# Kernel tuning notes

Measured on AMD Instinct MI355X. Metric: run time of the kernel, lower is better.

## Reference

```python
import jax, jax.numpy as jnp
import numpy as np

T1 = -0.075410217
T2 = 0.0
T3 = 0.062207676


def my_squash2(s_j):
    # s_j: [B, 1, C, O, 1]; piecewise-linear rescale based on sorted channel-0 magnitudes.
    B, _, C, O, _ = s_j.shape
    f = s_j[:, 0, :, 0, 0]                      # [B, C] first element of each capsule
    order = jnp.argsort(f, axis=1)
    srt = jnp.take_along_axis(f, order, axis=1)  # ascending sort per sample
    i1 = jnp.sum(srt < T1, axis=1, keepdims=True)
    i2 = jnp.sum(srt < T2, axis=1, keepdims=True)
    i3 = jnp.sum(srt < T3, axis=1, keepdims=True)
    pos = jnp.arange(C)[None, :]
    seg1 = -0.074520095 * srt + 0.349297946
    seg2 = -0.534473989 * srt + 0.27196494
    seg3 = 0.637642944 * srt + 0.295330779
    seg4 = 0.169344703 * srt + 0.353784456
    # faithful to torch slices [0:i1-1], [i1:i2-1], [i2:i3-1], [i3:9] (segment-end indices untouched)
    m1 = (i1 > 0) & (pos < i1 - 1)
    m2 = (i2 > 0) & (i2 > i1) & (pos >= i1) & (pos < i2 - 1)
    m3 = (i3 > 0) & (i3 > i2) & (pos >= i2) & (pos < i3 - 1)
    m4 = (i3 < C) & (pos >= i3) & (pos < C - 1)
    new_srt = jnp.where(m1, seg1, jnp.where(m2, seg2, jnp.where(m3, seg3, jnp.where(m4, seg4, srt))))
    inv = jnp.argsort(order, axis=1)
    new_f = jnp.take_along_axis(new_srt, inv, axis=1)  # unsort back to capsule order
    # torch code mutates s_j in place: channel 0 of each capsule becomes new_f
    s_mut = s_j.at[:, 0, :, 0, 0].set(new_f)
    scale = new_f[:, None, :, None, None]            # expanded over out_channels
    return scale * s_mut, s_mut


def setup_inputs() -> dict:
    key = jax.random.key(0)
    k0, k1, k2, k3 = jax.random.split(key, 4)
    B, R, C, O, I = 100, 1152, 10, 16, 8
    return {
        "x0": jax.random.normal(k0, (B, R, I), dtype=jnp.float32),
        "x1": jax.random.normal(k1, (B, R, I), dtype=jnp.float32),
        "x2": jax.random.normal(k2, (B, 1, 28, 28), dtype=jnp.float32),
        "W": jax.random.normal(k3, (1, R, C, O, I), dtype=jnp.float32),
        "train_or_test": 0,
        "epch": 0,
    }


def reference(x0, x1, x2, W, train_or_test, epch):
    B, R, I = x0.shape
    C, O = W.shape[2], W.shape[3]
    squashed_u = jnp.broadcast_to(x0[:, :, None, :, None], (B, R, C, I, 1))
    # u_hat[b,r,c,o] = sum_i W[0,r,c,o,i] * x0[b,r,i]
    u_hat = jnp.einsum('rcoi,bri->brco', W[0], x0)[..., None]  # [B,R,C,O,1]
    b_ij = jnp.zeros((1, R, C, 1), dtype=x0.dtype)
    num_iterations = 3
    for it in range(num_iterations):
        c_ij = jax.nn.softmax(b_ij, axis=1)                    # over routes
        c_full = jnp.broadcast_to(c_ij, (B, R, C, 1))[..., None]
        s_j = jnp.sum(c_full * u_hat, axis=1, keepdims=True)   # [B,1,C,O,1]
        v_j, s_mut = my_squash2(s_j)
        if it < num_iterations - 1:
            a = jnp.einsum('brco,bco->brc', u_hat[..., 0], v_j[:, 0, :, :, 0])
            b_ij = b_ij + jnp.mean(a, axis=0)[None, :, :, None]
    Wb = jnp.broadcast_to(W, (B,) + W.shape[1:])
    return (v_j[:, 0], c_full, Wb, squashed_u, x1, x2, s_mut[:, 0])
```

## Files before the change

kernel.cpp:

```cpp
#include <hip/hip_runtime.h>

#define B 100
#define R 1152
#define C 10
#define O 16
#define I 8
#define RI 9216
#define RC2 2304
#define RCHUNK 16
#define NRC 72
#define KCH 128

#define T1c (-0.075410217f)
#define T3c (0.062207676f)

typedef float f4raw __attribute__((ext_vector_type(4)));
static __device__ __forceinline__ void nt_store4(const float4& v, float4* p) {
    __builtin_nontemporal_store(*(const f4raw*)&v, (f4raw*)p);
}

#define WS_BCOL 0
#define WS_CSM  11520
#define WS_PART 23040
#define WS_VOB  1175040
#define WS_VBCO 1191040
#define WS_SMUT 1207040

#define O_VJ 0
#define O_CF 4000
#define O_WB 292000
#define O_SQ 37156000
#define O_X1 39460000
#define O_X2 39690400
#define O_SM 39710000

#define U_WB 7200
#define U_SQ 563
#define U_X1 57
#define U_X2 5
#define U_TOT 7825

__device__ void stream_unit(int u, const float4* __restrict__ W4,
                            const float4* __restrict__ x04,
                            const float4* __restrict__ x14,
                            const float4* __restrict__ x24,
                            float4* __restrict__ out) {
    const int t = threadIdx.x;
    if (u < U_WB) {
        int wchunk = u % 1440, bg = u / 1440;
        int idx = wchunk * 256 + t;
        float4 v = W4[idx];
        float4* dst = out + O_WB + (size_t)bg * 20 * 368640 + idx;
        #pragma unroll
        for (int b = 0; b < 20; b++) { nt_store4(v, dst); dst += 368640; }
    } else if (u < U_WB + U_SQ) {
        int s = u - U_WB;
        int m0 = s * 4096, m1 = m0 + 4096; if (m1 > 2304000) m1 = 2304000;
        for (int m = m0 + t; m < m1; m += 256) {
            float4 v = x04[(m / 20) * 2 + (m & 1)];
            nt_store4(v, &out[O_SQ + m]);
        }
    } else if (u < U_WB + U_SQ + U_X1) {
        int s = u - U_WB - U_SQ;
        int m0 = s * 4096, m1 = m0 + 4096; if (m1 > 230400) m1 = 230400;
        for (int m = m0 + t; m < m1; m += 256) nt_store4(x14[m], &out[O_X1 + m]);
    } else {
        int s = u - U_WB - U_SQ - U_X1;
        int m0 = s * 4096, m1 = m0 + 4096; if (m1 > 19600) m1 = 19600;
        for (int m = m0 + t; m < m1; m += 256) nt_store4(x24[m], &out[O_X2 + m]);
    }
}

__global__ __launch_bounds__(256) void k_gemm(const float* __restrict__ Wg,
                                              const float* __restrict__ x0,
                                              float* __restrict__ ws,
                                              const float4* __restrict__ x14,
                                              const float4* __restrict__ x24,
                                              float4* __restrict__ out,
                                              int it, int ubase) {
    const int t = threadIdx.x;
    const float4* x04 = (const float4*)x0;
    if (blockIdx.x >= 720) {
        int k = blockIdx.x - 720;
        #pragma unroll 1
        for (int n = 0; n < 3; n++)
            stream_unit(ubase + k * 3 + n, (const float4*)Wg, x04, x14, x24, out);
        return;
    }
    const int rc = blockIdx.x % NRC, c = blockIdx.x / NRC;
    const int r0 = rc * RCHUNK;
    __shared__ float red[256];
    __shared__ float cw[RCHUNK];
    __shared__ __align__(16) float lw[KCH * O];
    __shared__ float tp[64][104];

    if (it > 0) {
        const float* bcol = ws + WS_BCOL + c * R;
        float lm = -3.4e38f;
        for (int r = t; r < R; r += 256) lm = fmaxf(lm, bcol[r]);
        red[t] = lm; __syncthreads();
        for (int s = 128; s > 0; s >>= 1) { if (t < s) red[t] = fmaxf(red[t], red[t + s]); __syncthreads(); }
        const float m = red[0]; __syncthreads();
        float ls = 0.f;
        for (int r = t; r < R; r += 256) ls += expf(bcol[r] - m);
        red[t] = ls; __syncthreads();
        for (int s = 128; s > 0; s >>= 1) { if (t < s) red[t] += red[t + s]; __syncthreads(); }
        const float sinv = 1.f / red[0];
        if (t < RCHUNK) cw[t] = expf(bcol[r0 + t] - m) * sinv;
        if (it == 2 && rc == 0) {
            for (int r = t; r < R; r += 256)
                ws[WS_CSM + r * C + c] = expf(bcol[r] - m) * sinv;
        }
    } else {
        if (t < RCHUNK) cw[t] = 1.0f / 1152.0f;
    }
    __syncthreads();

    for (int j = t; j < KCH * O; j += 256) {
        int rr = j >> 7;
        int rem = j & 127;
        int o = rem >> 3, i = rem & 7;
        lw[((rr * I + i) << 4) + o] = cw[rr] * Wg[((size_t)(r0 + rr) * C + c) * 128 + rem];
    }

    const int bl = t & 63, og = t >> 6;
    int b2 = bl + 64; if (b2 > 103) b2 = 103;
    float4 a0 = {0, 0, 0, 0}, a1 = {0, 0, 0, 0};
    for (int p = 0; p < 2; p++) {
        __syncthreads();
        int colbase = r0 * 2 + p * 16;
        for (int e = t; e < 1600; e += 256) {
            int b = e >> 4, q = e & 15;
            float4 v = x04[(size_t)b * RC2 + colbase + q];
            tp[q * 4 + 0][b] = v.x; tp[q * 4 + 1][b] = v.y;
            tp[q * 4 + 2][b] = v.z; tp[q * 4 + 3][b] = v.w;
        }
        tp[t >> 2][100 + (t & 3)] = 0.f;
        __syncthreads();
        const float4* lwp = (const float4*)lw + p * 64 * 4;
        #pragma unroll 8
        for (int k = 0; k < 64; k++) {
            float xv0 = tp[k][bl];
            float xv1 = tp[k][b2];
            float4 wv = lwp[k * 4 + og];
            a0.x += xv0 * wv.x; a0.y += xv0 * wv.y; a0.z += xv0 * wv.z; a0.w += xv0 * wv.w;
            a1.x += xv1 * wv.x; a1.y += xv1 * wv.y; a1.z += xv1 * wv.z; a1.w += xv1 * wv.w;
        }
    }
    float4* part4 = (float4*)(ws + WS_PART);
    int base = ((c * NRC + rc) * B + bl) * 4 + og;
    part4[base] = a0;
    if (bl < 36) part4[base + 64 * 4] = a1;
}

__global__ __launch_bounds__(256) void k_squash(float* __restrict__ ws,
                                                const float* __restrict__ Wg,
                                                const float* __restrict__ x0,
                                                const float4* __restrict__ x14,
                                                const float4* __restrict__ x24,
                                                float4* __restrict__ out, int ubase) {
    const int t = threadIdx.x;
    if (blockIdx.x >= B) {
        int k = blockIdx.x - B;
        #pragma unroll 1
        for (int n = 0; n < 2; n++)
            stream_unit(ubase + k * 2 + n, (const float4*)Wg, (const float4*)x0, x14, x24, out);
        return;
    }
    const int b = blockIdx.x;
    __shared__ float sl[160];
    __shared__ float nf[C];
    if (t < 160) {
        int c = t >> 4, o = t & 15;
        float s = 0.f;
        const float* p = ws + WS_PART + ((size_t)c * NRC * B + b) * 16 + o;
        #pragma unroll 8
        for (int rc = 0; rc < NRC; rc++) s += p[rc * 1600];
        sl[t] = s;
    }
    __syncthreads();
    if (t < C) {
        float fv[C];
        #pragma unroll
        for (int c2 = 0; c2 < C; c2++) fv[c2] = sl[c2 * O];
        float mine = sl[t * O];
        int rank = 0, i1 = 0, i2 = 0, i3 = 0;
        #pragma unroll
        for (int c2 = 0; c2 < C; c2++) {
            rank += (fv[c2] < mine) || (fv[c2] == mine && c2 < t);
            i1 += fv[c2] < T1c;
            i2 += fv[c2] < 0.0f;
            i3 += fv[c2] < T3c;
        }
        float nv = mine;
        if (i1 > 0 && rank < i1 - 1)                               nv = -0.074520095f * mine + 0.349297946f;
        else if (i2 > 0 && i2 > i1 && rank >= i1 && rank < i2 - 1) nv = -0.534473989f * mine + 0.27196494f;
        else if (i3 > 0 && i3 > i2 && rank >= i2 && rank < i3 - 1) nv = 0.637642944f * mine + 0.295330779f;
        else if (i3 < C && rank >= i3 && rank < C - 1)             nv = 0.169344703f * mine + 0.353784456f;
        nf[t] = nv;
    }
    __syncthreads();
    if (t < 160) {
        int c = t >> 4, o = t & 15;
        float sv = sl[t];
        float nfv = nf[c];
        float smut = (o == 0) ? nfv : sv;
        float v = nfv * smut;
        ws[WS_VBCO + b * 160 + t] = v;
        ws[WS_SMUT + b * 160 + t] = smut;
        ws[WS_VOB + t * B + b] = v;
    }
}

__global__ __launch_bounds__(256) void k_agree(const float* __restrict__ Wg,
                                               const float* __restrict__ x0,
                                               float* __restrict__ ws,
                                               const float4* __restrict__ x14,
                                               const float4* __restrict__ x24,
                                               float4* __restrict__ out,
                                               int it, int ubase) {
    const int t = threadIdx.x;
    if (blockIdx.x >= R) {
        int k = blockIdx.x - R;
        #pragma unroll 1
        for (int n = 0; n < 3; n++)
            stream_unit(ubase + k * 3 + n, (const float4*)Wg, (const float4*)x0, x14, x24, out);
        return;
    }
    const int r = blockIdx.x;
    __shared__ __align__(16) float vt[3200];
    __shared__ __align__(16) float xs[800];
    __shared__ __align__(16) float arr[1280];
    const float4* x04 = (const float4*)x0;
    if (t < 200) {
        int b = t >> 1, half = t & 1;
        float4 v = x04[(size_t)b * RC2 + r * 2 + half];
        xs[(half * 4 + 0) * B + b] = v.x; xs[(half * 4 + 1) * B + b] = v.y;
        xs[(half * 4 + 2) * B + b] = v.z; xs[(half * 4 + 3) * B + b] = v.w;
    }
    const int i = t & 7, co0 = t >> 3;
    const float4* xs4 = (const float4*)(xs + i * B);
    const float4* vt4 = (const float4*)(vt + co0 * B);
    for (int ch = 0; ch < 5; ch++) {
        __syncthreads();
        for (int j = t; j < 3200; j += 256) vt[j] = ws[WS_VOB + ch * 3200 + j];
        __syncthreads();
        float q = 0.f;
        #pragma unroll
        for (int b4 = 0; b4 < 25; b4++) {
            float4 xv = xs4[b4];
            float4 vv = vt4[b4];
            q += xv.x * vv.x + xv.y * vv.y + xv.z * vv.z + xv.w * vv.w;
        }
        int co = ch * 32 + co0;
        arr[co * I + i] = q * Wg[(size_t)r * 1280 + co * I + i];
    }
    __syncthreads();
    if (t < C) {
        const float4* a4 = (const float4*)(arr + t * 128);
        float d = 0.f;
        #pragma unroll
        for (int m2 = 0; m2 < 32; m2++) { float4 v4 = a4[m2]; d += v4.x + v4.y + v4.z + v4.w; }
        float* dst = ws + WS_BCOL + t * R + r;
        float val = d * (1.0f / B);
        if (it == 0) *dst = val; else *dst += val;
    }
}

__global__ __launch_bounds__(256) void k_out(const float* __restrict__ x0,
                                             const float* __restrict__ x1,
                                             const float* __restrict__ x2,
                                             float* __restrict__ ws,
                                             const float* __restrict__ Wg,
                                             float4* __restrict__ out) {
    const int bid = blockIdx.x, t = threadIdx.x;
    const float4* cs4 = (const float4*)(ws + WS_CSM);
    const float4* vb4 = (const float4*)(ws + WS_VBCO);
    const float4* sm4 = (const float4*)(ws + WS_SMUT);
    for (int j = bid * 256 + t; j < 296000; j += 2048 * 256) {
        float4 v; int g;
        if (j < 4000)        { v = vb4[j]; g = j; }
        else if (j < 292000) { v = cs4[(j - 4000) % 2880]; g = j; }
        else                 { v = sm4[j - 292000]; g = O_SM + (j - 292000); }
        nt_store4(v, &out[g]);
    }
    if (bid < U_TOT - 6300)
        stream_unit(6300 + bid, (const float4*)Wg, (const float4*)x0,
                    (const float4*)x1, (const float4*)x2, out);
}

extern "C" void kernel_launch(void* const* d_in, const int* in_sizes, int n_in,
                              void* d_out, int out_size, void* d_ws, size_t ws_size,
                              hipStream_t stream) {
    (void)in_sizes; (void)n_in; (void)out_size; (void)ws_size;
    const float* x0 = (const float*)d_in[0];
    const float* x1 = (const float*)d_in[1];
    const float* x2 = (const float*)d_in[2];
    const float* Wg = (const float*)d_in[3];
    const float4* x14 = (const float4*)x1;
    const float4* x24 = (const float4*)x2;
    float* ws = (float*)d_ws;
    float4* out = (float4*)d_out;

    hipLaunchKernelGGL(k_gemm,   dim3(1020), dim3(256), 0, stream, Wg, x0, ws, x14, x24, out, 0, 0);
    hipLaunchKernelGGL(k_squash, dim3(400),  dim3(256), 0, stream, ws, Wg, x0, x14, x24, out, 900);
    hipLaunchKernelGGL(k_agree,  dim3(1452), dim3(256), 0, stream, Wg, x0, ws, x14, x24, out, 0, 1500);
    hipLaunchKernelGGL(k_gemm,   dim3(1020), dim3(256), 0, stream, Wg, x0, ws, x14, x24, out, 1, 2400);
    hipLaunchKernelGGL(k_squash, dim3(400),  dim3(256), 0, stream, ws, Wg, x0, x14, x24, out, 3300);
    hipLaunchKernelGGL(k_agree,  dim3(1452), dim3(256), 0, stream, Wg, x0, ws, x14, x24, out, 1, 3900);
    hipLaunchKernelGGL(k_gemm,   dim3(1020), dim3(256), 0, stream, Wg, x0, ws, x14, x24, out, 2, 4800);
    hipLaunchKernelGGL(k_squash, dim3(400),  dim3(256), 0, stream, ws, Wg, x0, x14, x24, out, 5700);
    hipLaunchKernelGGL(k_out,    dim3(2048), dim3(256), 0, stream, x0, x1, x2, ws, Wg, out);
}
```

Before: 227.0 us.

## Fold final squash into output kernel and rebalance streaming-copy units across launches

Drops the third k_squash launch and folds its per-sample reduction and squash into the first 100 blocks of k_out, which now write v_j and s_mut directly to the output. The earlier squash kernels no longer write the intermediate VBCO/SMUT buffers. The schedule of output-copy units is rebalanced: the earlier kernels get fewer streaming units (one per block) and k_out absorbs the rest, up to three per block. The GEMM inner loop reads x as float2 pairs, and k_agree loads v as float4. The intent is to cut one launch and some workspace traffic at the cost of a heavier final kernel, which may overlap less of the copy work with compute.

```diff
diff --git a/kernel.cpp b/kernel.cpp
--- a/kernel.cpp
+++ b/kernel.cpp
@@ -23,8 +23,6 @@
 #define WS_CSM  11520
 #define WS_PART 23040
 #define WS_VOB  1175040
-#define WS_VBCO 1191040
-#define WS_SMUT 1207040
 
 #define O_VJ 0
 #define O_CF 4000
@@ -37,7 +35,6 @@
 #define U_WB 7200
 #define U_SQ 563
 #define U_X1 57
-#define U_X2 5
 #define U_TOT 7825
 
 __device__ void stream_unit(int u, const float4* __restrict__ W4,
@@ -81,10 +78,7 @@
     const int t = threadIdx.x;
     const float4* x04 = (const float4*)x0;
     if (blockIdx.x >= 720) {
-        int k = blockIdx.x - 720;
-        #pragma unroll 1
-        for (int n = 0; n < 3; n++)
-            stream_unit(ubase + k * 3 + n, (const float4*)Wg, x04, x14, x24, out);
+        stream_unit(ubase + (blockIdx.x - 720), (const float4*)Wg, x04, x14, x24, out);
         return;
     }
     const int rc = blockIdx.x % NRC, c = blockIdx.x / NRC;
@@ -92,7 +86,7 @@
     __shared__ float red[256];
     __shared__ float cw[RCHUNK];
     __shared__ __align__(16) float lw[KCH * O];
-    __shared__ float tp[64][104];
+    __shared__ float2 tpp[32][104];
 
     if (it > 0) {
         const float* bcol = ws + WS_BCOL + c * R;
@@ -132,25 +126,32 @@
         for (int e = t; e < 1600; e += 256) {
             int b = e >> 4, q = e & 15;
             float4 v = x04[(size_t)b * RC2 + colbase + q];
-            tp[q * 4 + 0][b] = v.x; tp[q * 4 + 1][b] = v.y;
-            tp[q * 4 + 2][b] = v.z; tp[q * 4 + 3][b] = v.w;
-        }
-        tp[t >> 2][100 + (t & 3)] = 0.f;
-        __syncthreads();
-        const float4* lwp = (const float4*)lw + p * 64 * 4;
+            tpp[q * 2 + 0][b] = make_float2(v.x, v.y);
+            tpp[q * 2 + 1][b] = make_float2(v.z, v.w);
+        }
+        if (p == 0 && t < 128) tpp[t >> 2][100 + (t & 3)] = make_float2(0.f, 0.f);
+        __syncthreads();
+        const float4* lwp = (const float4*)lw + p * 256;
         #pragma unroll 8
-        for (int k = 0; k < 64; k++) {
-            float xv0 = tp[k][bl];
-            float xv1 = tp[k][b2];
-            float4 wv = lwp[k * 4 + og];
-            a0.x += xv0 * wv.x; a0.y += xv0 * wv.y; a0.z += xv0 * wv.z; a0.w += xv0 * wv.w;
-            a1.x += xv1 * wv.x; a1.y += xv1 * wv.y; a1.z += xv1 * wv.z; a1.w += xv1 * wv.w;
+        for (int k2 = 0; k2 < 32; k2++) {
+            float2 xv0 = tpp[k2][bl];
+            float2 xv1 = tpp[k2][b2];
+            float4 wa = lwp[(k2 * 2) * 4 + og];
+            float4 wb = lwp[(k2 * 2 + 1) * 4 + og];
+            a0.x += xv0.x * wa.x + xv0.y * wb.x;
+            a0.y += xv0.x * wa.y + xv0.y * wb.y;
+            a0.z += xv0.x * wa.z + xv0.y * wb.z;
+            a0.w += xv0.x * wa.w + xv0.y * wb.w;
+            a1.x += xv1.x * wa.x + xv1.y * wb.x;
+            a1.y += xv1.x * wa.y + xv1.y * wb.y;
+            a1.z += xv1.x * wa.z + xv1.y * wb.z;
+            a1.w += xv1.x * wa.w + xv1.y * wb.w;
         }
     }
     float4* part4 = (float4*)(ws + WS_PART);
     int base = ((c * NRC + rc) * B + bl) * 4 + og;
     part4[base] = a0;
-    if (bl < 36) part4[base + 64 * 4] = a1;
+    if (bl < 36) part4[base + 256] = a1;
 }
 
 __global__ __launch_bounds__(256) void k_squash(float* __restrict__ ws,
@@ -161,10 +162,7 @@
                                                 float4* __restrict__ out, int ubase) {
     const int t = threadIdx.x;
     if (blockIdx.x >= B) {
-        int k = blockIdx.x - B;
-        #pragma unroll 1
-        for (int n = 0; n < 2; n++)
-            stream_unit(ubase + k * 2 + n, (const float4*)Wg, (const float4*)x0, x14, x24, out);
+        stream_unit(ubase + (blockIdx.x - B), (const float4*)Wg, (const float4*)x0, x14, x24, out);
         return;
     }
     const int b = blockIdx.x;
@@ -202,13 +200,8 @@
     __syncthreads();
     if (t < 160) {
         int c = t >> 4, o = t & 15;
-        float sv = sl[t];
-        float nfv = nf[c];
-        float smut = (o == 0) ? nfv : sv;
-        float v = nfv * smut;
-        ws[WS_VBCO + b * 160 + t] = v;
-        ws[WS_SMUT + b * 160 + t] = smut;
-        ws[WS_VOB + t * B + b] = v;
+        float smut = (o == 0) ? nf[c] : sl[t];
+        ws[WS_VOB + t * B + b] = nf[c] * smut;
     }
 }
 
@@ -221,10 +214,7 @@
                                                int it, int ubase) {
     const int t = threadIdx.x;
     if (blockIdx.x >= R) {
-        int k = blockIdx.x - R;
-        #pragma unroll 1
-        for (int n = 0; n < 3; n++)
-            stream_unit(ubase + k * 3 + n, (const float4*)Wg, (const float4*)x0, x14, x24, out);
+        stream_unit(ubase + (blockIdx.x - R), (const float4*)Wg, (const float4*)x0, x14, x24, out);
         return;
     }
     const int r = blockIdx.x;
@@ -232,6 +222,7 @@
     __shared__ __align__(16) float xs[800];
     __shared__ __align__(16) float arr[1280];
     const float4* x04 = (const float4*)x0;
+    const float4* vob4 = (const float4*)(ws + WS_VOB);
     if (t < 200) {
         int b = t >> 1, half = t & 1;
         float4 v = x04[(size_t)b * RC2 + r * 2 + half];
@@ -241,9 +232,10 @@
     const int i = t & 7, co0 = t >> 3;
     const float4* xs4 = (const float4*)(xs + i * B);
     const float4* vt4 = (const float4*)(vt + co0 * B);
+    float4* vtw = (float4*)vt;
     for (int ch = 0; ch < 5; ch++) {
         __syncthreads();
-        for (int j = t; j < 3200; j += 256) vt[j] = ws[WS_VOB + ch * 3200 + j];
+        for (int j = t; j < 800; j += 256) vtw[j] = vob4[ch * 800 + j];
         __syncthreads();
         float q = 0.f;
         #pragma unroll
@@ -274,19 +266,63 @@
                                              const float* __restrict__ Wg,
                                              float4* __restrict__ out) {
     const int bid = blockIdx.x, t = threadIdx.x;
+    if (bid < B) {
+        const int b = bid;
+        __shared__ float sl[160];
+        __shared__ float nf[C];
+        __shared__ __align__(16) float vv[160];
+        __shared__ __align__(16) float sm[160];
+        if (t < 160) {
+            int c = t >> 4, o = t & 15;
+            float s = 0.f;
+            const float* p = ws + WS_PART + ((size_t)c * NRC * B + b) * 16 + o;
+            #pragma unroll 8
+            for (int rc = 0; rc < NRC; rc++) s += p[rc * 1600];
+            sl[t] = s;
+        }
+        __syncthreads();
+        if (t < C) {
+            float fv[C];
+            #pragma unroll
+            for (int c2 = 0; c2 < C; c2++) fv[c2] = sl[c2 * O];
+            float mine = sl[t * O];
+            int rank = 0, i1 = 0, i2 = 0, i3 = 0;
+            #pragma unroll
+            for (int c2 = 0; c2 < C; c2++) {
+                rank += (fv[c2] < mine) || (fv[c2] == mine && c2 < t);
+                i1 += fv[c2] < T1c;
+                i2 += fv[c2] < 0.0f;
+                i3 += fv[c2] < T3c;
+            }
+            float nv = mine;
+            if (i1 > 0 && rank < i1 - 1)                               nv = -0.074520095f * mine + 0.349297946f;
+            else if (i2 > 0 && i2 > i1 && rank >= i1 && rank < i2 - 1) nv = -0.534473989f * mine + 0.27196494f;
+            else if (i3 > 0 && i3 > i2 && rank >= i2 && rank < i3 - 1) nv = 0.637642944f * mine + 0.295330779f;
+            else if (i3 < C && rank >= i3 && rank < C - 1)             nv = 0.169344703f * mine + 0.353784456f;
+            nf[t] = nv;
+        }
+        __syncthreads();
+        if (t < 160) {
+            int c = t >> 4, o = t & 15;
+            float smut = (o == 0) ? nf[c] : sl[t];
+            sm[t] = smut;
+            vv[t] = nf[c] * smut;
+        }
+        __syncthreads();
+        if (t < 40) {
+            nt_store4(((const float4*)vv)[t], &out[O_VJ + b * 40 + t]);
+            nt_store4(((const float4*)sm)[t], &out[O_SM + b * 40 + t]);
+        }
+    }
     const float4* cs4 = (const float4*)(ws + WS_CSM);
-    const float4* vb4 = (const float4*)(ws + WS_VBCO);
-    const float4* sm4 = (const float4*)(ws + WS_SMUT);
-    for (int j = bid * 256 + t; j < 296000; j += 2048 * 256) {
-        float4 v; int g;
-        if (j < 4000)        { v = vb4[j]; g = j; }
-        else if (j < 292000) { v = cs4[(j - 4000) % 2880]; g = j; }
-        else                 { v = sm4[j - 292000]; g = O_SM + (j - 292000); }
-        nt_store4(v, &out[g]);
-    }
-    if (bid < U_TOT - 6300)
-        stream_unit(6300 + bid, (const float4*)Wg, (const float4*)x0,
-                    (const float4*)x1, (const float4*)x2, out);
+    for (int j = bid * 256 + t; j < 288000; j += 2048 * 256)
+        nt_store4(cs4[j % 2880], &out[O_CF + j]);
+    for (int k = 0; k < 3; k++) {
+        int u = 2700 + bid + k * 2048;
+        if (u < U_TOT)
+            stream_unit(u, (const float4*)Wg, (const float4*)x0,
+                        (const float4*)x1, (const float4*)x2, out);
+    }
 }
 
 extern "C" void kernel_launch(void* const* d_in, const int* in_sizes, int n_in,
@@ -302,13 +338,12 @@
     float* ws = (float*)d_ws;
     float4* out = (float4*)d_out;
 
-    hipLaunchKernelGGL(k_gemm,   dim3(1020), dim3(256), 0, stream, Wg, x0, ws, x14, x24, out, 0, 0);
-    hipLaunchKernelGGL(k_squash, dim3(400),  dim3(256), 0, stream, ws, Wg, x0, x14, x24, out, 900);
-    hipLaunchKernelGGL(k_agree,  dim3(1452), dim3(256), 0, stream, Wg, x0, ws, x14, x24, out, 0, 1500);
-    hipLaunchKernelGGL(k_gemm,   dim3(1020), dim3(256), 0, stream, Wg, x0, ws, x14, x24, out, 1, 2400);
-    hipLaunchKernelGGL(k_squash, dim3(400),  dim3(256), 0, stream, ws, Wg, x0, x14, x24, out, 3300);
-    hipLaunchKernelGGL(k_agree,  dim3(1452), dim3(256), 0, stream, Wg, x0, ws, x14, x24, out, 1, 3900);
-    hipLaunchKernelGGL(k_gemm,   dim3(1020), dim3(256), 0, stream, Wg, x0, ws, x14, x24, out, 2, 4800);
-    hipLaunchKernelGGL(k_squash, dim3(400),  dim3(256), 0, stream, ws, Wg, x0, x14, x24, out, 5700);
+    hipLaunchKernelGGL(k_gemm,   dim3(720 + 500), dim3(256), 0, stream, Wg, x0, ws, x14, x24, out, 0, 0);
+    hipLaunchKernelGGL(k_squash, dim3(100 + 200), dim3(256), 0, stream, ws, Wg, x0, x14, x24, out, 500);
+    hipLaunchKernelGGL(k_agree,  dim3(1152 + 400), dim3(256), 0, stream, Wg, x0, ws, x14, x24, out, 0, 700);
+    hipLaunchKernelGGL(k_gemm,   dim3(720 + 500), dim3(256), 0, stream, Wg, x0, ws, x14, x24, out, 1, 1100);
+    hipLaunchKernelGGL(k_squash, dim3(100 + 200), dim3(256), 0, stream, ws, Wg, x0, x14, x24, out, 1600);
+    hipLaunchKernelGGL(k_agree,  dim3(1152 + 400), dim3(256), 0, stream, Wg, x0, ws, x14, x24, out, 1, 1800);
+    hipLaunchKernelGGL(k_gemm,   dim3(720 + 500), dim3(256), 0, stream, Wg, x0, ws, x14, x24, out, 2, 2200);
     hipLaunchKernelGGL(k_out,    dim3(2048), dim3(256), 0, stream, x0, x1, x2, ws, Wg, out);
 }
```

After: 223.4 us. About the same (-1.6%).
